# Performance work log

Hardware: AMD Instinct MI355X
Metric: run time of the kernel (lower is better)

The kernel has to match this reference:

```python
import jax, jax.numpy as jnp
import numpy as np

N = 20000      # nodes
G = 400        # distinct TCR group ids
D_IN, H1, H2, D_OUT = 128, 256, 256, 128
LN_EPS = 1e-5


def _init_linear(key, fan_in, fan_out):
    s = 1.0 / np.sqrt(fan_in)
    return jax.random.uniform(key, (fan_in, fan_out), jnp.float32, -s, s)


def setup_inputs() -> dict:
    key = jax.random.key(0)
    ks = jax.random.split(key, 6)
    x = jax.random.normal(ks[0], (N, D_IN), jnp.float32)
    idx_TCR = jax.random.randint(ks[1], (N,), 0, G, dtype=jnp.int64)
    W1 = _init_linear(ks[2], D_IN, H1)
    W2 = _init_linear(ks[3], H1, H2)
    W3 = _init_linear(ks[4], H2, D_OUT)
    b1 = jnp.zeros((H1,), jnp.float32)
    b2 = jnp.zeros((H2,), jnp.float32)
    b3 = jnp.zeros((D_OUT,), jnp.float32)
    gamma = jnp.ones((D_OUT,), jnp.float32)
    beta = jnp.zeros((D_OUT,), jnp.float32)
    return {"x": x, "idx_TCR": idx_TCR, "W1": W1, "b1": b1,
            "W2": W2, "b2": b2, "W3": W3, "b3": b3,
            "gamma": gamma, "beta": beta}


def _build_edges(idx_TCR):
    # construct_graph: connect node pairs with equal idx, upper triangle only
    # (directed src<tgt edges, as in the torch code), then append self-loops
    # as PyG GCNConv.gcn_norm does.
    idx = np.asarray(idx_TCR).reshape(-1)
    n = idx.shape[0]
    eq = idx[:, None] == idx[None, :]
    src, tgt = np.nonzero(np.triu(eq, k=1))
    loop = np.arange(n)
    row = jnp.asarray(np.concatenate([src, loop]))  # message source
    col = jnp.asarray(np.concatenate([tgt, loop]))  # message target
    return row, col, n


def _gcn_norm(row, col, n, dtype):
    # degree from incoming edges (incl. self-loops), symmetric normalization
    deg = jax.ops.segment_sum(jnp.ones(row.shape[0], dtype), col, num_segments=n)
    dis = jnp.where(deg > 0, jax.lax.rsqrt(deg), jnp.zeros_like(deg))
    return dis[row] * dis[col]  # [E]


def _gcn_conv(x, W, b, row, col, norm, n):
    h = x @ W                                   # [N, out]
    msg = h[row] * norm[:, None]                # gather + scale, [E, out]
    out = jax.ops.segment_sum(msg, col, num_segments=n)  # scatter-add
    return out + b


def reference(x, idx_TCR, W1, b1, W2, b2, W3, b3, gamma, beta):
    row, col, n = _build_edges(idx_TCR)
    norm = _gcn_norm(row, col, n, x.dtype)
    h = jax.nn.relu(_gcn_conv(x, W1, b1, row, col, norm, n))
    h = jax.nn.relu(_gcn_conv(h, W2, b2, row, col, norm, n))
    h = jax.nn.relu(_gcn_conv(h, W3, b3, row, col, norm, n))
    # LayerNorm over last dim
    mu = h.mean(axis=-1, keepdims=True)
    var = ((h - mu) ** 2).mean(axis=-1, keepdims=True)
    return (h - mu) * jax.lax.rsqrt(var + LN_EPS) * gamma + beta
```

## Files before the change

kernel.cpp:

```cpp
#include <hip/hip_runtime.h>
#include <hip/hip_bf16.h>

#define NN 20000
#define NG 400
#define D_IN 128
#define H1 256
#define H2 256
#define D_OUT 128
#define WT_ELEMS (D_IN * H1 + H1 * H2 + H2 * D_OUT)
#define MC2 512
#define WSLOT 256

#define STY 72
#define ST1 136
#define ST2 264
#define ST3 264
#define SF  132
#define PIPEB 73728

typedef __attribute__((ext_vector_type(8))) short short8;
typedef __attribute__((ext_vector_type(4))) short short4v;
typedef __attribute__((ext_vector_type(4))) float floatx4;

__device__ __forceinline__ short f2b(float f) {
    __hip_bfloat16 h = __float2bfloat16(f);
    return *(short*)&h;
}


__global__ __launch_bounds__(256) void wt_all(
    const float* __restrict__ W1, const float* __restrict__ W2,
    const float* __restrict__ W3, __hip_bfloat16* __restrict__ Wt1,
    __hip_bfloat16* __restrict__ Wt2, __hip_bfloat16* __restrict__ Wt3)
{
    int o = blockIdx.x * 256 + threadIdx.x;
    if (o < D_IN * H1) {
        int n = o / D_IN, k = o - n * D_IN;
        Wt1[o] = __float2bfloat16(W1[(size_t)k * H1 + n]);
    } else if (o < D_IN * H1 + H1 * H2) {
        int p = o - D_IN * H1;
        int n = p / H1, k = p - n * H1;
        Wt2[p] = __float2bfloat16(W2[(size_t)k * H2 + n]);
    } else if (o < WT_ELEMS) {
        int p = o - D_IN * H1 - H1 * H2;
        int n = p / H2, k = p - n * H2;
        Wt3[p] = __float2bfloat16(W3[(size_t)k * D_OUT + n]);
    }
}


__global__ __launch_bounds__(512) void fused_gcn(
    const float* __restrict__ x, const int* __restrict__ idx,
    const __hip_bfloat16* __restrict__ Wt1_,
    const __hip_bfloat16* __restrict__ Wt2_,
    const __hip_bfloat16* __restrict__ Wt3_,
    const float* __restrict__ b1, const float* __restrict__ b2,
    const float* __restrict__ b3,
    const float* __restrict__ gamma, const float* __restrict__ beta,
    float* __restrict__ out)
{
    __shared__ __align__(16) char LB[2 * PIPEB];
    __shared__ int mlist0[MC2], mlist1[MC2];
    __shared__ int wcnt0[8], wcnt1[8];

    int tid = threadIdx.x;
    int w = tid >> 6;
    int lane = tid & 63;
    int quad = lane >> 4;
    int l15 = lane & 15;
    int p = w >> 2;
    int u = w & 3;
    int g0 = blockIdx.x * 2;
    int g1 = g0 + 1;

    int* WS0 = (int*)LB;
    int* WS1 = (int*)(LB + 8192);
    {
        int slice = w * 625;
        int wc0 = 0, wc1 = 0;
        unsigned long long lowm = (1ull << lane) - 1ull;
#pragma unroll
        for (int b2i = 0; b2i < 2; ++b2i) {
            int4 v[5];
#pragma unroll
            for (int r = 0; r < 5; ++r) {
                int q = (b2i * 5 + r) * 64 + lane;
                v[r] = (q < 625) ? *(const int4*)&idx[(slice + q) * 4]
                                 : make_int4(-1, -1, -1, -1);
            }
#pragma unroll
            for (int r = 0; r < 5; ++r) {
                int j0 = (slice + (b2i * 5 + r) * 64 + lane) * 4;
                {
                    bool f0 = (v[r].x == g0), f1 = (v[r].y == g0);
                    bool f2 = (v[r].z == g0), f3 = (v[r].w == g0);
                    unsigned long long m0 = __ballot(f0), m1 = __ballot(f1);
                    unsigned long long m2 = __ballot(f2), m3 = __ballot(f3);
                    int pp = wc0 + __popcll(m0 & lowm) + __popcll(m1 & lowm)
                                 + __popcll(m2 & lowm) + __popcll(m3 & lowm);
                    int e0 = (int)f0, e1 = (int)f1, e2 = (int)f2;
                    if (f0 && pp < WSLOT)                WS0[w * WSLOT + pp] = j0;
                    if (f1 && pp + e0 < WSLOT)           WS0[w * WSLOT + pp + e0] = j0 + 1;
                    if (f2 && pp + e0 + e1 < WSLOT)      WS0[w * WSLOT + pp + e0 + e1] = j0 + 2;
                    if (f3 && pp + e0 + e1 + e2 < WSLOT) WS0[w * WSLOT + pp + e0 + e1 + e2] = j0 + 3;
                    wc0 += __popcll(m0) + __popcll(m1) + __popcll(m2) + __popcll(m3);
                }
                {
                    bool f0 = (v[r].x == g1), f1 = (v[r].y == g1);
                    bool f2 = (v[r].z == g1), f3 = (v[r].w == g1);
                    unsigned long long m0 = __ballot(f0), m1 = __ballot(f1);
                    unsigned long long m2 = __ballot(f2), m3 = __ballot(f3);
                    int pp = wc1 + __popcll(m0 & lowm) + __popcll(m1 & lowm)
                                 + __popcll(m2 & lowm) + __popcll(m3 & lowm);
                    int e0 = (int)f0, e1 = (int)f1, e2 = (int)f2;
                    if (f0 && pp < WSLOT)                WS1[w * WSLOT + pp] = j0;
                    if (f1 && pp + e0 < WSLOT)           WS1[w * WSLOT + pp + e0] = j0 + 1;
                    if (f2 && pp + e0 + e1 < WSLOT)      WS1[w * WSLOT + pp + e0 + e1] = j0 + 2;
                    if (f3 && pp + e0 + e1 + e2 < WSLOT) WS1[w * WSLOT + pp + e0 + e1 + e2] = j0 + 3;
                    wc1 += __popcll(m0) + __popcll(m1) + __popcll(m2) + __popcll(m3);
                }
            }
        }
        if (lane == 0) { wcnt0[w] = min(wc0, WSLOT); wcnt1[w] = min(wc1, WSLOT); }
    }
    __syncthreads();
    int cnt0 = 0, cnt1 = 0;
    {
        int pre0 = 0, pre1 = 0;
#pragma unroll
        for (int ww = 0; ww < 8; ++ww) {
            int c0 = wcnt0[ww], c1w = wcnt1[ww];
            if (ww < w) { pre0 += c0; pre1 += c1w; }
            cnt0 += c0; cnt1 += c1w;
        }
        cnt0 = min(cnt0, MC2); cnt1 = min(cnt1, MC2);
        int myc0 = wcnt0[w], myc1 = wcnt1[w];
        for (int k = lane; k < myc0; k += 64) {
            int dstp = pre0 + k;
            if (dstp < MC2) mlist0[dstp] = WS0[w * WSLOT + k];
        }
        for (int k = lane; k < myc1; k += 64) {
            int dstp = pre1 + k;
            if (dstp < MC2) mlist1[dstp] = WS1[w * WSLOT + k];
        }
    }
    int cmax = max(cnt0, cnt1);
    if (cmax <= 0) return;

    float2 gmv = *(const float2*)&gamma[lane * 2];
    float2 btv = *(const float2*)&beta[lane * 2];

    __syncthreads();

    int mycnt = p ? cnt1 : cnt0;
    int* mylist = p ? mlist1 : mlist0;
    char* PB = LB + p * PIPEB;

    auto ltfrag = [&](int nt, int k2) -> short8 {
        int thr = nt * 16 + l15 - k2 * 32 - quad * 8;
        short8 f;
#pragma unroll
        for (int e = 0; e < 8; ++e)
            f[e] = (e <= thr) ? (short)0x3F80 : (short)0;
        return f;
    };

    float c1[2][2][4], c2[2][2][4], c3[2][4];
#pragma unroll
    for (int hf = 0; hf < 2; ++hf)
#pragma unroll
        for (int r = 0; r < 4; ++r) {
            c1[hf][0][r] = 0.f; c1[hf][1][r] = 0.f;
            c2[hf][0][r] = 0.f; c2[hf][1][r] = 0.f;
            c3[hf][r] = 0.f;
        }

    const short* wt1p = (const short*)Wt1_;
    const short* wt2p = (const short*)Wt2_;
    const short* wt3p = (const short*)Wt3_;

    for (int base = 0; base < cmax; base += 64) {
        asm("" : "+s"(wt1p), "+s"(wt2p), "+s"(wt3p));
        int mt = min(64, mycnt - base);
        int par = (base >> 6) & 1;
        char* Rc = PB + (par ? 36864 : 0);
        char* Rd = PB + (par ? 0 : 36864);
        short* T1 = (short*)Rc;
        short* T2 = (short*)Rc;
        short* T3 = (short*)Rc;
        float* F  = (float*)Rc;
        short* Yt = (short*)Rd;

        float djn[4];
#pragma unroll
        for (int nt = 0; nt < 4; ++nt)
            djn[nt] = rsqrtf((float)(base + nt * 16 + l15 + 1));

#pragma unroll
        for (int hf = 0; hf < 2; ++hf) {
            int hw = hf * 4 + u;
            int row = (lane >> 3) + 8 * hw;
            int mr = base + row;
            int mi = (mr < mycnt) ? mr : (mycnt > 0 ? mycnt - 1 : 0);
            int nid = (mycnt > 0) ? mylist[mi] : 0;
            float sdr = rsqrtf((float)(mr + 1));
            const float* xp = x + (size_t)nid * D_IN + (lane & 7) * 4;
#pragma unroll
            for (int t = 0; t < 4; ++t) {
                float4 v = *(const float4*)(xp + t * 32);
                short4v o;
                o[0] = f2b(v.x * sdr); o[1] = f2b(v.y * sdr);
                o[2] = f2b(v.z * sdr); o[3] = f2b(v.w * sdr);
                *(short4v*)&T1[row * ST1 + (lane & 7) * 4 + t * 32] = o;
            }
        }
        __syncthreads();

#pragma unroll
        for (int hf = 0; hf < 2; ++hf) {
            int hw = hf * 4 + u;
            floatx4 acc[4][2];
#pragma unroll
            for (int i = 0; i < 4; ++i) { acc[i][0] = (floatx4)0.0f; acc[i][1] = (floatx4)0.0f; }
#pragma unroll
            for (int kk = 0; kk < 4; ++kk) {
                short8 a4[4], bw[2];
#pragma unroll
                for (int i = 0; i < 4; ++i)
                    a4[i] = *(const short8*)&T1[(i * 16 + l15) * ST1 + kk * 32 + quad * 8];
#pragma unroll
                for (int nt = 0; nt < 2; ++nt)
                    bw[nt] = *(const short8*)&wt1p[((size_t)((hw * 2 + nt) * 16 + l15)) * D_IN + kk * 32 + quad * 8];
#pragma unroll
                for (int i = 0; i < 4; ++i)
#pragma unroll
                    for (int nt = 0; nt < 2; ++nt)
                        acc[i][nt] = __builtin_amdgcn_mfma_f32_16x16x32_bf16(
                            a4[i], bw[nt], acc[i][nt], 0, 0, 0);
            }
#pragma unroll
            for (int i = 0; i < 4; ++i)
#pragma unroll
                for (int nt = 0; nt < 2; ++nt) {
                    short4v o4;
#pragma unroll
                    for (int r = 0; r < 4; ++r) o4[r] = f2b(acc[i][nt][r]);
                    *(short4v*)&Yt[((hw * 2 + nt) * 16 + l15) * STY + i * 16 + quad * 4] = o4;
                }
        }
        __syncthreads();

#pragma unroll
        for (int hf = 0; hf < 2; ++hf) {
            int hw = hf * 4 + u;
            floatx4 acc[2][4];
#pragma unroll
            for (int i = 0; i < 2; ++i)
#pragma unroll
                for (int nt = 0; nt < 4; ++nt) acc[i][nt] = (floatx4)0.0f;
#pragma unroll
            for (int k2 = 0; k2 < 2; ++k2) {
                short8 af[2];
#pragma unroll
                for (int i = 0; i < 2; ++i)
                    af[i] = *(const short8*)&Yt[((2 * hw + i) * 16 + l15) * STY + k2 * 32 + quad * 8];
#pragma unroll
                for (int nt = 0; nt < 4; ++nt) {
                    short8 lt = ltfrag(nt, k2);
#pragma unroll
                    for (int i = 0; i < 2; ++i)
                        acc[i][nt] = __builtin_amdgcn_mfma_f32_16x16x32_bf16(
                            af[i], lt, acc[i][nt], 0, 0, 0);
                }
            }
#pragma unroll
            for (int i = 0; i < 2; ++i) {
                float4 bb = *(const float4*)&b1[(2 * hw + i) * 16 + quad * 4];
                float nc[4] = {0.f, 0.f, 0.f, 0.f};
#pragma unroll
                for (int nt = 0; nt < 4; ++nt) {
                    float tmp[4];
#pragma unroll
                    for (int r = 0; r < 4; ++r) tmp[r] = acc[i][nt][r] + c1[hf][i][r];
                    if (nt == 3) {
#pragma unroll
                        for (int r = 0; r < 4; ++r) nc[r] = tmp[r];
                    }
                    short4v o4;
                    o4[0] = f2b(fmaxf(tmp[0] * djn[nt] + bb.x, 0.0f) * djn[nt]);
                    o4[1] = f2b(fmaxf(tmp[1] * djn[nt] + bb.y, 0.0f) * djn[nt]);
                    o4[2] = f2b(fmaxf(tmp[2] * djn[nt] + bb.z, 0.0f) * djn[nt]);
                    o4[3] = f2b(fmaxf(tmp[3] * djn[nt] + bb.w, 0.0f) * djn[nt]);
                    *(short4v*)&T2[(nt * 16 + l15) * ST2 + (2 * hw + i) * 16 + quad * 4] = o4;
                }
#pragma unroll
                for (int r = 0; r < 4; ++r)
                    c1[hf][i][r] = __shfl(nc[r], (lane & 48) + 15);
            }
        }
        __syncthreads();

#pragma unroll
        for (int hf = 0; hf < 2; ++hf) {
            int hw = hf * 4 + u;
            floatx4 acc[4][2];
#pragma unroll
            for (int i = 0; i < 4; ++i) { acc[i][0] = (floatx4)0.0f; acc[i][1] = (floatx4)0.0f; }
#pragma unroll
            for (int kk = 0; kk < 8; ++kk) {
                short8 a4[4], bw[2];
#pragma unroll
                for (int i = 0; i < 4; ++i)
                    a4[i] = *(const short8*)&T2[(i * 16 + l15) * ST2 + kk * 32 + quad * 8];
#pragma unroll
                for (int nt = 0; nt < 2; ++nt)
                    bw[nt] = *(const short8*)&wt2p[((size_t)((hw * 2 + nt) * 16 + l15)) * H1 + kk * 32 + quad * 8];
#pragma unroll
                for (int i = 0; i < 4; ++i)
#pragma unroll
                    for (int nt = 0; nt < 2; ++nt)
                        acc[i][nt] = __builtin_amdgcn_mfma_f32_16x16x32_bf16(
                            a4[i], bw[nt], acc[i][nt], 0, 0, 0);
            }
#pragma unroll
            for (int i = 0; i < 4; ++i)
#pragma unroll
                for (int nt = 0; nt < 2; ++nt) {
                    short4v o4;
#pragma unroll
                    for (int r = 0; r < 4; ++r) o4[r] = f2b(acc[i][nt][r]);
                    *(short4v*)&Yt[((hw * 2 + nt) * 16 + l15) * STY + i * 16 + quad * 4] = o4;
                }
        }
        __syncthreads();

#pragma unroll
        for (int hf = 0; hf < 2; ++hf) {
            int hw = hf * 4 + u;
            floatx4 acc[2][4];
#pragma unroll
            for (int i = 0; i < 2; ++i)
#pragma unroll
                for (int nt = 0; nt < 4; ++nt) acc[i][nt] = (floatx4)0.0f;
#pragma unroll
            for (int k2 = 0; k2 < 2; ++k2) {
                short8 af[2];
#pragma unroll
                for (int i = 0; i < 2; ++i)
                    af[i] = *(const short8*)&Yt[((2 * hw + i) * 16 + l15) * STY + k2 * 32 + quad * 8];
#pragma unroll
                for (int nt = 0; nt < 4; ++nt) {
                    short8 lt = ltfrag(nt, k2);
#pragma unroll
                    for (int i = 0; i < 2; ++i)
                        acc[i][nt] = __builtin_amdgcn_mfma_f32_16x16x32_bf16(
                            af[i], lt, acc[i][nt], 0, 0, 0);
                }
            }
#pragma unroll
            for (int i = 0; i < 2; ++i) {
                float4 bb = *(const float4*)&b2[(2 * hw + i) * 16 + quad * 4];
                float nc[4] = {0.f, 0.f, 0.f, 0.f};
#pragma unroll
                for (int nt = 0; nt < 4; ++nt) {
                    float tmp[4];
#pragma unroll
                    for (int r = 0; r < 4; ++r) tmp[r] = acc[i][nt][r] + c2[hf][i][r];
                    if (nt == 3) {
#pragma unroll
                        for (int r = 0; r < 4; ++r) nc[r] = tmp[r];
                    }
                    short4v o4;
                    o4[0] = f2b(fmaxf(tmp[0] * djn[nt] + bb.x, 0.0f) * djn[nt]);
                    o4[1] = f2b(fmaxf(tmp[1] * djn[nt] + bb.y, 0.0f) * djn[nt]);
                    o4[2] = f2b(fmaxf(tmp[2] * djn[nt] + bb.z, 0.0f) * djn[nt]);
                    o4[3] = f2b(fmaxf(tmp[3] * djn[nt] + bb.w, 0.0f) * djn[nt]);
                    *(short4v*)&T3[(nt * 16 + l15) * ST3 + (2 * hw + i) * 16 + quad * 4] = o4;
                }
#pragma unroll
                for (int r = 0; r < 4; ++r)
                    c2[hf][i][r] = __shfl(nc[r], (lane & 48) + 15);
            }
        }
        __syncthreads();

#pragma unroll
        for (int hf = 0; hf < 2; ++hf) {
            int hw = hf * 4 + u;
            floatx4 acc[4];
#pragma unroll
            for (int i = 0; i < 4; ++i) acc[i] = (floatx4)0.0f;
#pragma unroll
            for (int kk = 0; kk < 8; ++kk) {
                short8 bw = *(const short8*)&wt3p[((size_t)(hw * 16 + l15)) * H2 + kk * 32 + quad * 8];
#pragma unroll
                for (int i = 0; i < 4; ++i) {
                    short8 a4 = *(const short8*)&T3[(i * 16 + l15) * ST3 + kk * 32 + quad * 8];
                    acc[i] = __builtin_amdgcn_mfma_f32_16x16x32_bf16(a4, bw, acc[i], 0, 0, 0);
                }
            }
#pragma unroll
            for (int i = 0; i < 4; ++i) {
                short4v o4;
#pragma unroll
                for (int r = 0; r < 4; ++r) o4[r] = f2b(acc[i][r]);
                *(short4v*)&Yt[(hw * 16 + l15) * STY + i * 16 + quad * 4] = o4;
            }
        }
        __syncthreads();

#pragma unroll
        for (int hf = 0; hf < 2; ++hf) {
            int hw = hf * 4 + u;
            floatx4 acc[4];
#pragma unroll
            for (int nt = 0; nt < 4; ++nt) acc[nt] = (floatx4)0.0f;
#pragma unroll
            for (int k2 = 0; k2 < 2; ++k2) {
                short8 af = *(const short8*)&Yt[(hw * 16 + l15) * STY + k2 * 32 + quad * 8];
#pragma unroll
                for (int nt = 0; nt < 4; ++nt)
                    acc[nt] = __builtin_amdgcn_mfma_f32_16x16x32_bf16(
                        af, ltfrag(nt, k2), acc[nt], 0, 0, 0);
            }
            float4 bb = *(const float4*)&b3[hw * 16 + quad * 4];
            float nc[4] = {0.f, 0.f, 0.f, 0.f};
#pragma unroll
            for (int nt = 0; nt < 4; ++nt) {
                float tmp[4];
#pragma unroll
                for (int r = 0; r < 4; ++r) tmp[r] = acc[nt][r] + c3[hf][r];
                if (nt == 3) {
#pragma unroll
                    for (int r = 0; r < 4; ++r) nc[r] = tmp[r];
                }
                float4 o;
                o.x = fmaxf(tmp[0] * djn[nt] + bb.x, 0.0f);
                o.y = fmaxf(tmp[1] * djn[nt] + bb.y, 0.0f);
                o.z = fmaxf(tmp[2] * djn[nt] + bb.z, 0.0f);
                o.w = fmaxf(tmp[3] * djn[nt] + bb.w, 0.0f);
                *(float4*)&F[(nt * 16 + l15) * SF + hw * 16 + quad * 4] = o;
            }
#pragma unroll
            for (int r = 0; r < 4; ++r)
                c3[hf][r] = __shfl(nc[r], (lane & 48) + 15);
        }
        __syncthreads();

#pragma unroll
        for (int hf = 0; hf < 2; ++hf) {
            int hw = hf * 4 + u;
            for (int r = hw; r < mt; r += 8) {
                float2 v = *(const float2*)&F[r * SF + lane * 2];
                float s1 = v.x + v.y;
                float s2v = v.x * v.x + v.y * v.y;
#pragma unroll
                for (int off = 32; off > 0; off >>= 1) {
                    s1 += __shfl_down(s1, off);
                    s2v += __shfl_down(s2v, off);
                }
                s1 = __shfl(s1, 0);
                s2v = __shfl(s2v, 0);
                float mu = s1 * (1.0f / D_OUT);
                float var = s2v * (1.0f / D_OUT) - mu * mu;
                float rstd = rsqrtf(var + 1e-5f);
                float2 o;
                o.x = (v.x - mu) * rstd * gmv.x + btv.x;
                o.y = (v.y - mu) * rstd * gmv.y + btv.y;
                *(float2*)&out[(size_t)mylist[base + r] * D_OUT + lane * 2] = o;
            }
        }
    }
}


extern "C" void kernel_launch(void* const* d_in, const int* in_sizes, int n_in,
                              void* d_out, int out_size, void* d_ws, size_t ws_size,
                              hipStream_t stream) {
    const float* x     = (const float*)d_in[0];
    const int*   idx   = (const int*)d_in[1];
    const float* W1    = (const float*)d_in[2];
    const float* b1    = (const float*)d_in[3];
    const float* W2    = (const float*)d_in[4];
    const float* b2    = (const float*)d_in[5];
    const float* W3    = (const float*)d_in[6];
    const float* b3    = (const float*)d_in[7];
    const float* gamma = (const float*)d_in[8];
    const float* beta  = (const float*)d_in[9];
    float* out = (float*)d_out;

    char* ws = (char*)d_ws;
    size_t off = 0;
    auto alloc = [&](size_t bytes) -> void* {
        void* p = (void*)(ws + off);
        off += (bytes + 255) & ~(size_t)255;
        return p;
    };
    __hip_bfloat16* Wt1 = (__hip_bfloat16*)alloc((size_t)D_IN * H1 * 2);
    __hip_bfloat16* Wt2 = (__hip_bfloat16*)alloc((size_t)H1 * H2 * 2);
    __hip_bfloat16* Wt3 = (__hip_bfloat16*)alloc((size_t)H2 * D_OUT * 2);

    wt_all<<<(WT_ELEMS + 255) / 256, 256, 0, stream>>>(
        W1, W2, W3, Wt1, Wt2, Wt3);

    fused_gcn<<<NG / 2, 512, 0, stream>>>(
        x, idx, Wt1, Wt2, Wt3, b1, b2, b3, gamma, beta, out);
}
```

Before: 134.9 us.

## Double block size to 1024 threads, one output slice per wave

Blocks grow from 512 to 1024 threads, so each group is handled by 8 waves and each wave covers a single slice of output columns, where before 4 waves each looped over two halves. Only 200 blocks run on a device with many CUs, so this puts more waves in flight per group and shortens the serial per-wave work. Bias vectors are now hoisted into registers before the main loop. The cost is larger blocks that require launch_bounds(1024) to fit in the register budget, plus more waves waiting at each barrier.

```diff
diff --git a/kernel.cpp b/kernel.cpp
--- a/kernel.cpp
+++ b/kernel.cpp
@@ -16,7 +16,8 @@
 #define ST2 264
 #define ST3 264
 #define SF  132
-#define PIPEB 73728
+#define REGB 36864
+#define PIPEB (2 * REGB)
 
 typedef __attribute__((ext_vector_type(8))) short short8;
 typedef __attribute__((ext_vector_type(4))) short short4v;
@@ -49,7 +50,7 @@
 }
 
 
-__global__ __launch_bounds__(512) void fused_gcn(
+__global__ __launch_bounds__(1024, 4) void fused_gcn(
     const float* __restrict__ x, const int* __restrict__ idx,
     const __hip_bfloat16* __restrict__ Wt1_,
     const __hip_bfloat16* __restrict__ Wt2_,
@@ -68,14 +69,14 @@
     int lane = tid & 63;
     int quad = lane >> 4;
     int l15 = lane & 15;
-    int p = w >> 2;
-    int u = w & 3;
+    int p = w >> 3;
+    int u = w & 7;
     int g0 = blockIdx.x * 2;
     int g1 = g0 + 1;
 
     int* WS0 = (int*)LB;
     int* WS1 = (int*)(LB + 8192);
-    {
+    if (w < 8) {
         int slice = w * 625;
         int wc0 = 0, wc1 = 0;
         unsigned long long lowm = (1ull << lane) - 1ull;
@@ -134,14 +135,16 @@
             cnt0 += c0; cnt1 += c1w;
         }
         cnt0 = min(cnt0, MC2); cnt1 = min(cnt1, MC2);
-        int myc0 = wcnt0[w], myc1 = wcnt1[w];
-        for (int k = lane; k < myc0; k += 64) {
-            int dstp = pre0 + k;
-            if (dstp < MC2) mlist0[dstp] = WS0[w * WSLOT + k];
-        }
-        for (int k = lane; k < myc1; k += 64) {
-            int dstp = pre1 + k;
-            if (dstp < MC2) mlist1[dstp] = WS1[w * WSLOT + k];
+        if (w < 8) {
+            int myc0 = wcnt0[w], myc1 = wcnt1[w];
+            for (int k = lane; k < myc0; k += 64) {
+                int dstp = pre0 + k;
+                if (dstp < MC2) mlist0[dstp] = WS0[w * WSLOT + k];
+            }
+            for (int k = lane; k < myc1; k += 64) {
+                int dstp = pre1 + k;
+                if (dstp < MC2) mlist1[dstp] = WS1[w * WSLOT + k];
+            }
         }
     }
     int cmax = max(cnt0, cnt1);
@@ -149,6 +152,13 @@
 
     float2 gmv = *(const float2*)&gamma[lane * 2];
     float2 btv = *(const float2*)&beta[lane * 2];
+    float4 bb1[2], bb2[2], bb3;
+#pragma unroll
+    for (int i = 0; i < 2; ++i) {
+        bb1[i] = *(const float4*)&b1[(2 * u + i) * 16 + quad * 4];
+        bb2[i] = *(const float4*)&b2[(2 * u + i) * 16 + quad * 4];
+    }
+    bb3 = *(const float4*)&b3[u * 16 + quad * 4];
 
     __syncthreads();
 
@@ -165,15 +175,13 @@
         return f;
     };
 
-    float c1[2][2][4], c2[2][2][4], c3[2][4];
-#pragma unroll
-    for (int hf = 0; hf < 2; ++hf)
-#pragma unroll
-        for (int r = 0; r < 4; ++r) {
-            c1[hf][0][r] = 0.f; c1[hf][1][r] = 0.f;
-            c2[hf][0][r] = 0.f; c2[hf][1][r] = 0.f;
-            c3[hf][r] = 0.f;
-        }
+    float c1[2][4], c2[2][4], c3[4];
+#pragma unroll
+    for (int r = 0; r < 4; ++r) {
+        c1[0][r] = 0.f; c1[1][r] = 0.f;
+        c2[0][r] = 0.f; c2[1][r] = 0.f;
+        c3[r] = 0.f;
+    }
 
     const short* wt1p = (const short*)Wt1_;
     const short* wt2p = (const short*)Wt2_;
@@ -183,8 +191,8 @@
         asm("" : "+s"(wt1p), "+s"(wt2p), "+s"(wt3p));
         int mt = min(64, mycnt - base);
         int par = (base >> 6) & 1;
-        char* Rc = PB + (par ? 36864 : 0);
-        char* Rd = PB + (par ? 0 : 36864);
+        char* Rc = PB + (par ? REGB : 0);
+        char* Rd = PB + (par ? 0 : REGB);
         short* T1 = (short*)Rc;
         short* T2 = (short*)Rc;
         short* T3 = (short*)Rc;
@@ -196,10 +204,8 @@
         for (int nt = 0; nt < 4; ++nt)
             djn[nt] = rsqrtf((float)(base + nt * 16 + l15 + 1));
 
-#pragma unroll
-        for (int hf = 0; hf < 2; ++hf) {
-            int hw = hf * 4 + u;
-            int row = (lane >> 3) + 8 * hw;
+        {
+            int row = (lane >> 3) + 8 * u;
             int mr = base + row;
             int mi = (mr < mycnt) ? mr : (mycnt > 0 ? mycnt - 1 : 0);
             int nid = (mycnt > 0) ? mylist[mi] : 0;
@@ -216,9 +222,7 @@
         }
         __syncthreads();
 
-#pragma unroll
-        for (int hf = 0; hf < 2; ++hf) {
-            int hw = hf * 4 + u;
+        {
             floatx4 acc[4][2];
 #pragma unroll
             for (int i = 0; i < 4; ++i) { acc[i][0] = (floatx4)0.0f; acc[i][1] = (floatx4)0.0f; }
@@ -230,7 +234,7 @@
                     a4[i] = *(const short8*)&T1[(i * 16 + l15) * ST1 + kk * 32 + quad * 8];
 #pragma unroll
                 for (int nt = 0; nt < 2; ++nt)
-                    bw[nt] = *(const short8*)&wt1p[((size_t)((hw * 2 + nt) * 16 + l15)) * D_IN + kk * 32 + quad * 8];
+                    bw[nt] = *(const short8*)&wt1p[((size_t)((u * 2 + nt) * 16 + l15)) * D_IN + kk * 32 + quad * 8];
 #pragma unroll
                 for (int i = 0; i < 4; ++i)
 #pragma unroll
@@ -245,14 +249,12 @@
                     short4v o4;
 #pragma unroll
                     for (int r = 0; r < 4; ++r) o4[r] = f2b(acc[i][nt][r]);
-                    *(short4v*)&Yt[((hw * 2 + nt) * 16 + l15) * STY + i * 16 + quad * 4] = o4;
-                }
-        }
-        __syncthreads();
-
-#pragma unroll
-        for (int hf = 0; hf < 2; ++hf) {
-            int hw = hf * 4 + u;
+                    *(short4v*)&Yt[((u * 2 + nt) * 16 + l15) * STY + i * 16 + quad * 4] = o4;
+                }
+        }
+        __syncthreads();
+
+        {
             floatx4 acc[2][4];
 #pragma unroll
             for (int i = 0; i < 2; ++i)
@@ -263,7 +265,7 @@
                 short8 af[2];
 #pragma unroll
                 for (int i = 0; i < 2; ++i)
-                    af[i] = *(const short8*)&Yt[((2 * hw + i) * 16 + l15) * STY + k2 * 32 + quad * 8];
+                    af[i] = *(const short8*)&Yt[((2 * u + i) * 16 + l15) * STY + k2 * 32 + quad * 8];
 #pragma unroll
                 for (int nt = 0; nt < 4; ++nt) {
                     short8 lt = ltfrag(nt, k2);
@@ -275,34 +277,31 @@
             }
 #pragma unroll
             for (int i = 0; i < 2; ++i) {
-                float4 bb = *(const float4*)&b1[(2 * hw + i) * 16 + quad * 4];
                 float nc[4] = {0.f, 0.f, 0.f, 0.f};
 #pragma unroll
                 for (int nt = 0; nt < 4; ++nt) {
                     float tmp[4];
 #pragma unroll
-                    for (int r = 0; r < 4; ++r) tmp[r] = acc[i][nt][r] + c1[hf][i][r];
+                    for (int r = 0; r < 4; ++r) tmp[r] = acc[i][nt][r] + c1[i][r];
                     if (nt == 3) {
 #pragma unroll
                         for (int r = 0; r < 4; ++r) nc[r] = tmp[r];
                     }
                     short4v o4;
-                    o4[0] = f2b(fmaxf(tmp[0] * djn[nt] + bb.x, 0.0f) * djn[nt]);
-                    o4[1] = f2b(fmaxf(tmp[1] * djn[nt] + bb.y, 0.0f) * djn[nt]);
-                    o4[2] = f2b(fmaxf(tmp[2] * djn[nt] + bb.z, 0.0f) * djn[nt]);
-                    o4[3] = f2b(fmaxf(tmp[3] * djn[nt] + bb.w, 0.0f) * djn[nt]);
-                    *(short4v*)&T2[(nt * 16 + l15) * ST2 + (2 * hw + i) * 16 + quad * 4] = o4;
+                    o4[0] = f2b(fmaxf(tmp[0] * djn[nt] + bb1[i].x, 0.0f) * djn[nt]);
+                    o4[1] = f2b(fmaxf(tmp[1] * djn[nt] + bb1[i].y, 0.0f) * djn[nt]);
+                    o4[2] = f2b(fmaxf(tmp[2] * djn[nt] + bb1[i].z, 0.0f) * djn[nt]);
+                    o4[3] = f2b(fmaxf(tmp[3] * djn[nt] + bb1[i].w, 0.0f) * djn[nt]);
+                    *(short4v*)&T2[(nt * 16 + l15) * ST2 + (2 * u + i) * 16 + quad * 4] = o4;
                 }
 #pragma unroll
                 for (int r = 0; r < 4; ++r)
-                    c1[hf][i][r] = __shfl(nc[r], (lane & 48) + 15);
-            }
-        }
-        __syncthreads();
-
-#pragma unroll
-        for (int hf = 0; hf < 2; ++hf) {
-            int hw = hf * 4 + u;
+                    c1[i][r] = __shfl(nc[r], (lane & 48) + 15);
+            }
+        }
+        __syncthreads();
+
+        {
             floatx4 acc[4][2];
 #pragma unroll
             for (int i = 0; i < 4; ++i) { acc[i][0] = (floatx4)0.0f; acc[i][1] = (floatx4)0.0f; }
@@ -314,7 +313,7 @@
                     a4[i] = *(const short8*)&T2[(i * 16 + l15) * ST2 + kk * 32 + quad * 8];
 #pragma unroll
                 for (int nt = 0; nt < 2; ++nt)
-                    bw[nt] = *(const short8*)&wt2p[((size_t)((hw * 2 + nt) * 16 + l15)) * H1 + kk * 32 + quad * 8];
+                    bw[nt] = *(const short8*)&wt2p[((size_t)((u * 2 + nt) * 16 + l15)) * H1 + kk * 32 + quad * 8];
 #pragma unroll
                 for (int i = 0; i < 4; ++i)
 #pragma unroll
@@ -329,14 +328,12 @@
                     short4v o4;
 #pragma unroll
                     for (int r = 0; r < 4; ++r) o4[r] = f2b(acc[i][nt][r]);
-                    *(short4v*)&Yt[((hw * 2 + nt) * 16 + l15) * STY + i * 16 + quad * 4] = o4;
-                }
-        }
-        __syncthreads();
-
-#pragma unroll
-        for (int hf = 0; hf < 2; ++hf) {
-            int hw = hf * 4 + u;
+                    *(short4v*)&Yt[((u * 2 + nt) * 16 + l15) * STY + i * 16 + quad * 4] = o4;
+                }
+        }
+        __syncthreads();
+
+        {
             floatx4 acc[2][4];
 #pragma unroll
             for (int i = 0; i < 2; ++i)
@@ -347,7 +344,7 @@
                 short8 af[2];
 #pragma unroll
                 for (int i = 0; i < 2; ++i)
-                    af[i] = *(const short8*)&Yt[((2 * hw + i) * 16 + l15) * STY + k2 * 32 + quad * 8];
+                    af[i] = *(const short8*)&Yt[((2 * u + i) * 16 + l15) * STY + k2 * 32 + quad * 8];
 #pragma unroll
                 for (int nt = 0; nt < 4; ++nt) {
                     short8 lt = ltfrag(nt, k2);
@@ -359,40 +356,37 @@
             }
 #pragma unroll
             for (int i = 0; i < 2; ++i) {
-                float4 bb = *(const float4*)&b2[(2 * hw + i) * 16 + quad * 4];
                 float nc[4] = {0.f, 0.f, 0.f, 0.f};
 #pragma unroll
                 for (int nt = 0; nt < 4; ++nt) {
                     float tmp[4];
 #pragma unroll
-                    for (int r = 0; r < 4; ++r) tmp[r] = acc[i][nt][r] + c2[hf][i][r];
+                    for (int r = 0; r < 4; ++r) tmp[r] = acc[i][nt][r] + c2[i][r];
                     if (nt == 3) {
 #pragma unroll
                         for (int r = 0; r < 4; ++r) nc[r] = tmp[r];
                     }
                     short4v o4;
-                    o4[0] = f2b(fmaxf(tmp[0] * djn[nt] + bb.x, 0.0f) * djn[nt]);
-                    o4[1] = f2b(fmaxf(tmp[1] * djn[nt] + bb.y, 0.0f) * djn[nt]);
-                    o4[2] = f2b(fmaxf(tmp[2] * djn[nt] + bb.z, 0.0f) * djn[nt]);
-                    o4[3] = f2b(fmaxf(tmp[3] * djn[nt] + bb.w, 0.0f) * djn[nt]);
-                    *(short4v*)&T3[(nt * 16 + l15) * ST3 + (2 * hw + i) * 16 + quad * 4] = o4;
+                    o4[0] = f2b(fmaxf(tmp[0] * djn[nt] + bb2[i].x, 0.0f) * djn[nt]);
+                    o4[1] = f2b(fmaxf(tmp[1] * djn[nt] + bb2[i].y, 0.0f) * djn[nt]);
+                    o4[2] = f2b(fmaxf(tmp[2] * djn[nt] + bb2[i].z, 0.0f) * djn[nt]);
+                    o4[3] = f2b(fmaxf(tmp[3] * djn[nt] + bb2[i].w, 0.0f) * djn[nt]);
+                    *(short4v*)&T3[(nt * 16 + l15) * ST3 + (2 * u + i) * 16 + quad * 4] = o4;
                 }
 #pragma unroll
                 for (int r = 0; r < 4; ++r)
-                    c2[hf][i][r] = __shfl(nc[r], (lane & 48) + 15);
-            }
-        }
-        __syncthreads();
-
-#pragma unroll
-        for (int hf = 0; hf < 2; ++hf) {
-            int hw = hf * 4 + u;
+                    c2[i][r] = __shfl(nc[r], (lane & 48) + 15);
+            }
+        }
+        __syncthreads();
+
+        {
             floatx4 acc[4];
 #pragma unroll
             for (int i = 0; i < 4; ++i) acc[i] = (floatx4)0.0f;
 #pragma unroll
             for (int kk = 0; kk < 8; ++kk) {
-                short8 bw = *(const short8*)&wt3p[((size_t)(hw * 16 + l15)) * H2 + kk * 32 + quad * 8];
+                short8 bw = *(const short8*)&wt3p[((size_t)(u * 16 + l15)) * H2 + kk * 32 + quad * 8];
 #pragma unroll
                 for (int i = 0; i < 4; ++i) {
                     short8 a4 = *(const short8*)&T3[(i * 16 + l15) * ST3 + kk * 32 + quad * 8];
@@ -404,71 +398,64 @@
                 short4v o4;
 #pragma unroll
                 for (int r = 0; r < 4; ++r) o4[r] = f2b(acc[i][r]);
-                *(short4v*)&Yt[(hw * 16 + l15) * STY + i * 16 + quad * 4] = o4;
-            }
-        }
-        __syncthreads();
-
-#pragma unroll
-        for (int hf = 0; hf < 2; ++hf) {
-            int hw = hf * 4 + u;
+                *(short4v*)&Yt[(u * 16 + l15) * STY + i * 16 + quad * 4] = o4;
+            }
+        }
+        __syncthreads();
+
+        {
             floatx4 acc[4];
 #pragma unroll
             for (int nt = 0; nt < 4; ++nt) acc[nt] = (floatx4)0.0f;
 #pragma unroll
             for (int k2 = 0; k2 < 2; ++k2) {
-                short8 af = *(const short8*)&Yt[(hw * 16 + l15) * STY + k2 * 32 + quad * 8];
+                short8 af = *(const short8*)&Yt[(u * 16 + l15) * STY + k2 * 32 + quad * 8];
 #pragma unroll
                 for (int nt = 0; nt < 4; ++nt)
                     acc[nt] = __builtin_amdgcn_mfma_f32_16x16x32_bf16(
                         af, ltfrag(nt, k2), acc[nt], 0, 0, 0);
             }
-            float4 bb = *(const float4*)&b3[hw * 16 + quad * 4];
             float nc[4] = {0.f, 0.f, 0.f, 0.f};
 #pragma unroll
             for (int nt = 0; nt < 4; ++nt) {
                 float tmp[4];
 #pragma unroll
-                for (int r = 0; r < 4; ++r) tmp[r] = acc[nt][r] + c3[hf][r];
+                for (int r = 0; r < 4; ++r) tmp[r] = acc[nt][r] + c3[r];
                 if (nt == 3) {
 #pragma unroll
                     for (int r = 0; r < 4; ++r) nc[r] = tmp[r];
                 }
                 float4 o;
-                o.x = fmaxf(tmp[0] * djn[nt] + bb.x, 0.0f);
-                o.y = fmaxf(tmp[1] * djn[nt] + bb.y, 0.0f);
-                o.z = fmaxf(tmp[2] * djn[nt] + bb.z, 0.0f);
-                o.w = fmaxf(tmp[3] * djn[nt] + bb.w, 0.0f);
-                *(float4*)&F[(nt * 16 + l15) * SF + hw * 16 + quad * 4] = o;
+                o.x = fmaxf(tmp[0] * djn[nt] + bb3.x, 0.0f);
+                o.y = fmaxf(tmp[1] * djn[nt] + bb3.y, 0.0f);
+                o.z = fmaxf(tmp[2] * djn[nt] + bb3.z, 0.0f);
+                o.w = fmaxf(tmp[3] * djn[nt] + bb3.w, 0.0f);
+                *(float4*)&F[(nt * 16 + l15) * SF + u * 16 + quad * 4] = o;
             }
 #pragma unroll
             for (int r = 0; r < 4; ++r)
-                c3[hf][r] = __shfl(nc[r], (lane & 48) + 15);
-        }
-        __syncthreads();
-
-#pragma unroll
-        for (int hf = 0; hf < 2; ++hf) {
-            int hw = hf * 4 + u;
-            for (int r = hw; r < mt; r += 8) {
-                float2 v = *(const float2*)&F[r * SF + lane * 2];
-                float s1 = v.x + v.y;
-                float s2v = v.x * v.x + v.y * v.y;
-#pragma unroll
-                for (int off = 32; off > 0; off >>= 1) {
-                    s1 += __shfl_down(s1, off);
-                    s2v += __shfl_down(s2v, off);
-                }
-                s1 = __shfl(s1, 0);
-                s2v = __shfl(s2v, 0);
-                float mu = s1 * (1.0f / D_OUT);
-                float var = s2v * (1.0f / D_OUT) - mu * mu;
-                float rstd = rsqrtf(var + 1e-5f);
-                float2 o;
-                o.x = (v.x - mu) * rstd * gmv.x + btv.x;
-                o.y = (v.y - mu) * rstd * gmv.y + btv.y;
-                *(float2*)&out[(size_t)mylist[base + r] * D_OUT + lane * 2] = o;
-            }
+                c3[r] = __shfl(nc[r], (lane & 48) + 15);
+        }
+        __syncthreads();
+
+        for (int r = u; r < mt; r += 8) {
+            float2 v = *(const float2*)&F[r * SF + lane * 2];
+            float s1 = v.x + v.y;
+            float s2v = v.x * v.x + v.y * v.y;
+#pragma unroll
+            for (int off = 32; off > 0; off >>= 1) {
+                s1 += __shfl_down(s1, off);
+                s2v += __shfl_down(s2v, off);
+            }
+            s1 = __shfl(s1, 0);
+            s2v = __shfl(s2v, 0);
+            float mu = s1 * (1.0f / D_OUT);
+            float var = s2v * (1.0f / D_OUT) - mu * mu;
+            float rstd = rsqrtf(var + 1e-5f);
+            float2 o;
+            o.x = (v.x - mu) * rstd * gmv.x + btv.x;
+            o.y = (v.y - mu) * rstd * gmv.y + btv.y;
+            *(float2*)&out[(size_t)mylist[base + r] * D_OUT + lane * 2] = o;
         }
     }
 }
@@ -503,6 +490,6 @@
     wt_all<<<(WT_ELEMS + 255) / 256, 256, 0, stream>>>(
         W1, W2, W3, Wt1, Wt2, Wt3);
 
-    fused_gcn<<<NG / 2, 512, 0, stream>>>(
+    fused_gcn<<<NG / 2, 1024, 0, stream>>>(
         x, idx, Wt1, Wt2, Wt3, b1, b2, b3, gamma, beta, out);
 }
```

New measurement: 153.3 us. +13.6%, slower.
